# Optimization experiments

Hardware: AMD Instinct MI355X
Metric: run time of the kernel (lower is better)

Reference implementation:

```python
import jax, jax.numpy as jnp
import numpy as np

L = 24        # n_layer
E = 1024      # n_emb
H = 4 * E     # ffn hidden
V = 50277     # vocab
LN_EPS = 1e-5


def _ln(x, w, b):
    m = x.mean(-1, keepdims=True)
    v = ((x - m) ** 2).mean(-1, keepdims=True)
    return (x - m) / jnp.sqrt(v + LN_EPS) * w + b


def setup_inputs() -> dict:
    key = jax.random.key(0)
    ks = jax.random.split(key, 24)
    s = 1.0 / np.sqrt(E)      # keep matvec outputs O(1) so exp-recurrence is stable
    sh = 1.0 / np.sqrt(H)
    inp = {
        "emb":      jax.random.normal(ks[0], (V, E), jnp.float32) * 0.02,
        "ln0_w":    jnp.ones((E,), jnp.float32),
        "ln0_b":    jnp.zeros((E,), jnp.float32),
        "ln1_w":    jnp.ones((L, E), jnp.float32),
        "ln1_b":    jnp.zeros((L, E), jnp.float32),
        "att_tmk":  jax.random.uniform(ks[1], (L, E), jnp.float32),
        "att_tmv":  jax.random.uniform(ks[2], (L, E), jnp.float32),
        "att_tmr":  jax.random.uniform(ks[3], (L, E), jnp.float32),
        "att_tf":   jax.random.normal(ks[4], (L, E), jnp.float32) * 0.3,
        # checkpoint stores raw time_decay; loader applies -exp(.)
        "att_td":   -jnp.exp(jax.random.normal(ks[5], (L, E), jnp.float32) * 0.3),
        "att_kw":   jax.random.normal(ks[6], (L, E, E), jnp.float32) * s,
        "att_vw":   jax.random.normal(ks[7], (L, E, E), jnp.float32) * s,
        "att_rw":   jax.random.normal(ks[8], (L, E, E), jnp.float32) * s,
        "att_ow":   jax.random.normal(ks[9], (L, E, E), jnp.float32) * s,
        "ln2_w":    jnp.ones((L, E), jnp.float32),
        "ln2_b":    jnp.zeros((L, E), jnp.float32),
        "ffn_tmk":  jax.random.uniform(ks[10], (L, E), jnp.float32),
        "ffn_tmr":  jax.random.uniform(ks[11], (L, E), jnp.float32),
        "ffn_kw":   jax.random.normal(ks[12], (L, H, E), jnp.float32) * s,
        "ffn_vw":   jax.random.normal(ks[13], (L, E, H), jnp.float32) * sh,
        "ffn_rw":   jax.random.normal(ks[14], (L, E, E), jnp.float32) * s,
        "ln_out_w": jnp.ones((E,), jnp.float32),
        "ln_out_b": jnp.zeros((E,), jnp.float32),
        "head_w":   jax.random.normal(ks[15], (V, E), jnp.float32) * s,
        "token":    123,
    }
    state = jnp.zeros((5 * L, E), jnp.float32)
    state = state.at[4::5].set(-1e30)  # pp slot, as in empty_state()
    inp["state"] = state
    return inp


def _rwkv_forward(emb, ln0_w, ln0_b, ln1_w, ln1_b, att_tmk, att_tmv, att_tmr,
                  att_tf, att_td, att_kw, att_vw, att_rw, att_ow,
                  ln2_w, ln2_b, ffn_tmk, ffn_tmr, ffn_kw, ffn_vw, ffn_rw,
                  ln_out_w, ln_out_b, head_w, state, token):
    x = emb[token]
    x = _ln(x, ln0_w, ln0_b)           # blocks.0.ln0 applied once before layer 0
    st = state.reshape(L, 5, E)        # slots: (ffn_x, att_x, aa, bb, pp)

    def step(x, inp):
        (s, l1w, l1b, tmk, tmv, tmr, tf, td, kw, vw, rw, ow,
         l2w, l2b, ftmk, ftmr, fkw, fvw, frw) = inp
        ffn_x, att_x, aa, bb, pp = s[0], s[1], s[2], s[3], s[4]
        # --- time-mix (SA) ---
        xn = _ln(x, l1w, l1b)
        xk = xn * tmk + att_x * (1 - tmk)
        xv = xn * tmv + att_x * (1 - tmv)
        xr = xn * tmr + att_x * (1 - tmr)
        r = jax.nn.sigmoid(rw @ xr)
        k = kw @ xk
        v = vw @ xv
        # numerically-stabilized WKV output
        ww = tf + k
        p = jnp.maximum(pp, ww)
        e1 = jnp.exp(pp - p)
        e2 = jnp.exp(ww - p)
        a = e1 * aa + e2 * v
        b = e1 * bb + e2
        # state update
        ww2 = pp + td
        p2 = jnp.maximum(ww2, k)
        f1 = jnp.exp(ww2 - p2)
        f2 = jnp.exp(k - p2)
        naa = f1 * aa + f2 * v
        nbb = f1 * bb + f2
        npp = p2
        sx = x + ow @ (r * a / b)
        # --- channel-mix (FF) ---
        xn2 = _ln(sx, l2w, l2b)
        fxk = xn2 * ftmk + ffn_x * (1 - ftmk)
        fxr = xn2 * ftmr + ffn_x * (1 - ftmr)
        fr = jax.nn.sigmoid(frw @ fxr)
        fk = jnp.square(jax.nn.relu(fkw @ fxk))
        out = sx + fr * (fvw @ fk)
        new_s = jnp.stack([xn2, xn, naa, nbb, npp])
        return out, new_s

    xs = (st, ln1_w, ln1_b, att_tmk, att_tmv, att_tmr, att_tf, att_td,
          att_kw, att_vw, att_rw, att_ow, ln2_w, ln2_b, ffn_tmk, ffn_tmr,
          ffn_kw, ffn_vw, ffn_rw)
    x, new_st = jax.lax.scan(step, x, xs)
    logits = head_w @ _ln(x, ln_out_w, ln_out_b)
    return logits, new_st.reshape(5 * L, E)


def reference(emb, ln0_w, ln0_b, ln1_w, ln1_b, att_tmk, att_tmv, att_tmr,
              att_tf, att_td, att_kw, att_vw, att_rw, att_ow,
              ln2_w, ln2_b, ffn_tmk, ffn_tmr, ffn_kw, ffn_vw, ffn_rw,
              ln_out_w, ln_out_b, head_w, state, token):
    return _rwkv_forward(emb, ln0_w, ln0_b, ln1_w, ln1_b, att_tmk, att_tmv,
                         att_tmr, att_tf, att_td, att_kw, att_vw, att_rw,
                         att_ow, ln2_w, ln2_b, ffn_tmk, ffn_tmr, ffn_kw,
                         ffn_vw, ffn_rw, ln_out_w, ln_out_b, head_w,
                         state, token)
```

## Files before the change

kernel.cpp:

```cpp
#include <hip/hip_runtime.h>

#define E 1024
#define H 4096
#define NLAYER 24
#define V 50277
#define NB 256
#define NT 1024
#define LN_EPS 1e-5f

typedef unsigned long long u64;

#define R1O    0
#define R2O    16384
#define POOLO  32768
#define SXO    36864
#define SSXO   37888
#define FXRO   38912
#define REDO   39936
#define PARTO  39968
#define PART2O 39984
#define SMEMF  40000

struct Params {
  const float* emb;   const float* ln0_w; const float* ln0_b;
  const float* ln1_w; const float* ln1_b;
  const float* tmk;   const float* tmv;   const float* tmr;
  const float* tf;    const float* td;
  const float* kw;    const float* vw;    const float* rw;  const float* ow;
  const float* ln2_w; const float* ln2_b;
  const float* ftmk;  const float* ftmr;
  const float* fkw;   const float* fvw;   const float* frw;
  const float* lnow;  const float* lnob;  const float* headw;
  const float* st;    const int* tok;
  float* out; float* ws;
};

__device__ __forceinline__ void stg_tag(u64* p, float v, unsigned tag) {
  u64 w = ((u64)__float_as_uint(v) << 32) | (u64)tag;
  __hip_atomic_store(p, w, __ATOMIC_RELAXED, __HIP_MEMORY_SCOPE_AGENT);
}
__device__ __forceinline__ u64 ld_tag(const u64* p) {
  return __hip_atomic_load(p, __ATOMIC_RELAXED, __HIP_MEMORY_SCOPE_AGENT);
}
__device__ __forceinline__ float poll_tag(const u64* p, unsigned tag) {
  u64 w = ld_tag(p);
  while ((unsigned)w != tag) { __builtin_amdgcn_s_sleep(1); w = ld_tag(p); }
  return __uint_as_float((unsigned)(w >> 32));
}

__device__ __forceinline__ void wait_pf() {
  asm volatile("s_waitcnt vmcnt(0)" ::: "memory");
}

__device__ __forceinline__ void gload_lds16(const float* g, float* l) {
  __builtin_amdgcn_global_load_lds(
      (const __attribute__((address_space(1))) unsigned int*)(g),
      (__attribute__((address_space(3))) unsigned int*)(l), 16, 0, 0);
}
__device__ __forceinline__ void pf_row4k(const float* row, float* dst, int lane) {
#pragma unroll
  for (int c = 0; c < 4; ++c)
    gload_lds16(row + c * 256 + lane * 4, dst + c * 256);
}

__device__ __forceinline__ float warp_sum(float v) {
#pragma unroll
  for (int off = 32; off; off >>= 1) v += __shfl_down(v, off);
  return v;
}

__device__ __forceinline__ float2 ln_stats(float v, float* red) {
  float a = v, b = v * v;
#pragma unroll
  for (int off = 32; off; off >>= 1) { a += __shfl_xor(a, off); b += __shfl_xor(b, off); }
  const int wid = threadIdx.x >> 6, lane = threadIdx.x & 63;
  if (lane == 0) { red[2 * wid] = a; red[2 * wid + 1] = b; }
  __syncthreads();
  float s1 = 0.f, s2 = 0.f;
  const float2* r2 = (const float2*)red;
#pragma unroll
  for (int j = 0; j < 16; ++j) { float2 t = r2[j]; s1 += t.x; s2 += t.y; }
  float m = s1 * (1.f / E);
  return make_float2(m, s2 * (1.f / E) - m * m);
}

__device__ __forceinline__ float dot4(float4 a, float4 b) {
  return a.x * b.x + a.y * b.y + a.z * b.z + a.w * b.w;
}

__device__ __forceinline__ float dotlds(const float* wrow, const float* vec, int lane) {
  const float4* w4 = (const float4*)wrow;
  const float4* v4 = (const float4*)vec;
  float acc = 0.f;
#pragma unroll
  for (int p = 0; p < 4; ++p)
    acc += dot4(w4[lane + p * 64], v4[lane + p * 64]);
  return warp_sum(acc);
}

__device__ __forceinline__ float dot1024(const float* __restrict__ Wrow,
                                         const float* vec, int lane) {
  const float4* W4 = (const float4*)Wrow;
  const float4* v4 = (const float4*)vec;
  float acc = 0.f;
#pragma unroll
  for (int p = 0; p < 4; ++p)
    acc += dot4(W4[lane + p * 64], v4[lane + p * 64]);
  return warp_sum(acc);
}

__global__ __launch_bounds__(NT, 1) void rwkv_kernel(Params p) {
  const int tid = threadIdx.x, bid = blockIdx.x;
  const int lane = tid & 63, wid = tid >> 6;

  extern __shared__ float smem[];
  float* r1     = smem + R1O;
  float* r2     = smem + R2O;
  float* pool   = smem + POOLO;
  float* s_x    = smem + SXO;
  float* s_sx   = smem + SSXO;
  float* s_fxr  = smem + FXRO;
  float* s_red  = smem + REDO;
  float* s_part = smem + PARTO;
  float* s_part2= smem + PART2O;

  u64* tws = (u64*)p.ws;
  u64* tk  = tws;
  u64* tv  = tws + 2 * E;
  u64* tr  = tws + 4 * E;
  u64* tsx = tws + 6 * E;
  u64* tx  = tws + 8 * E;
  u64* tfk = tws + 10 * E;

  float* out_st = p.out + V;
  const int token = p.tok[0];

  const bool hasA = wid < 12;
  const int rA = bid * 12 + wid;
  const int matA = rA >> 10, rmA = rA & (E - 1);
  const int rloc = wid >> 2, kc = wid & 3;
  const int rowO = bid * 4 + rloc;
  float* wA = r1 + wid * 1024;
  float* wD = r2 + wid * 1024;

  if (hasA) {
    const float* W = (matA == 0 ? p.kw : matA == 1 ? p.vw : p.rw) + (size_t)rmA * E;
    pf_row4k(W, wA, lane);
  }

  {
    float v = p.emb[(size_t)token * E + tid];
    float2 mv = ln_stats(v, s_red);
    s_x[tid] = (v - mv.x) / sqrtf(mv.y + LN_EPS) * p.ln0_w[tid] + p.ln0_b[tid];
  }

  for (int l = 0; l < NLAYER; ++l) {
    const float* stl = p.st + (size_t)5 * l * E;
    float* ostl = out_st + (size_t)5 * l * E;
    const int par = l & 1;
    const unsigned tg = (unsigned)(l + 1);

    float xv_;
    if (l > 0) { xv_ = poll_tag(&tx[par * E + tid], (unsigned)l); s_x[tid] = xv_; }
    else       { xv_ = s_x[tid]; }
    {
      float2 mv = ln_stats(xv_, s_red);
      float xn = (xv_ - mv.x) / sqrtf(mv.y + LN_EPS) * p.ln1_w[l * E + tid] + p.ln1_b[l * E + tid];
      float ax = stl[E + tid];
      float a = p.tmk[l * E + tid], b = p.tmv[l * E + tid], c = p.tmr[l * E + tid];
      pool[tid]        = xn * a + ax * (1.f - a);
      pool[1024 + tid] = xn * b + ax * (1.f - b);
      pool[2048 + tid] = xn * c + ax * (1.f - c);
      if (bid == 0) ostl[E + tid] = xn;
    }
    __syncthreads();
    wait_pf();
    if (hasA) {
      float d = dotlds(wA, pool + matA * 1024, lane);
      if (lane == 0) {
        u64* dst = (matA == 0 ? tk : matA == 1 ? tv : tr) + par * E + rmA;
        stg_tag(dst, matA == 2 ? 1.f / (1.f + expf(-d)) : d, tg);
      }
    }

    float4 wow = ((const float4*)(p.ow + (size_t)l * E * E + (size_t)rowO * E + kc * 256))[lane];
    pf_row4k(p.fkw + (size_t)l * H * E + (size_t)(bid * 16 + wid) * E, wA, lane);
    {
      const u64 *bk = tk + par * E + tid, *bv = tv + par * E + tid, *br = tr + par * E + tid;
      u64 wk = ld_tag(bk), wv = ld_tag(bv), wr = ld_tag(br);
      while ((unsigned)wk != tg) { __builtin_amdgcn_s_sleep(1); wk = ld_tag(bk); }
      while ((unsigned)wv != tg) { __builtin_amdgcn_s_sleep(1); wv = ld_tag(bv); }
      while ((unsigned)wr != tg) { __builtin_amdgcn_s_sleep(1); wr = ld_tag(br); }
      float kk = __uint_as_float((unsigned)(wk >> 32));
      float vv = __uint_as_float((unsigned)(wv >> 32));
      float rr = __uint_as_float((unsigned)(wr >> 32));
      float aav = stl[2 * E + tid], bbv = stl[3 * E + tid], ppv = stl[4 * E + tid];
      float tfv = p.tf[l * E + tid], tdv = p.td[l * E + tid];
      float wwv = tfv + kk;
      float pm = fmaxf(ppv, wwv);
      float e1 = expf(ppv - pm), e2 = expf(wwv - pm);
      float a = e1 * aav + e2 * vv, b = e1 * bbv + e2;
      pool[3072 + tid] = rr * a / b;
      float ww2 = ppv + tdv;
      float p2 = fmaxf(ww2, kk);
      float f1 = expf(ww2 - p2), f2 = expf(kk - p2);
      if (bid == 0) {
        ostl[2 * E + tid] = f1 * aav + f2 * vv;
        ostl[3 * E + tid] = f1 * bbv + f2;
        ostl[4 * E + tid] = p2;
      }
    }
    __syncthreads();
    {
      const float4* v4 = (const float4*)(pool + 3072 + kc * 256);
      float acc = warp_sum(dot4(wow, v4[lane]));
      if (lane == 0) s_part[wid] = acc;
    }
    __syncthreads();
    if (tid < 4) {
      float dsum = s_part[tid * 4] + s_part[tid * 4 + 1] +
                   s_part[tid * 4 + 2] + s_part[tid * 4 + 3];
      stg_tag(&tsx[par * E + bid * 4 + tid], s_x[bid * 4 + tid] + dsum, tg);
    }

    {
      float sxv = poll_tag(&tsx[par * E + tid], tg);
      s_sx[tid] = sxv;
      float4 wfr = ((const float4*)(p.frw + (size_t)l * E * E + (size_t)rowO * E + kc * 256))[lane];
      pf_row4k(p.fvw + (size_t)l * E * H + (size_t)rowO * H + kc * 1024, wD, lane);
      float2 mv = ln_stats(sxv, s_red);
      float xn2 = (sxv - mv.x) / sqrtf(mv.y + LN_EPS) * p.ln2_w[l * E + tid] + p.ln2_b[l * E + tid];
      float fx = stl[tid];
      float a = p.ftmk[l * E + tid], b = p.ftmr[l * E + tid];
      pool[tid]  = xn2 * a + fx * (1.f - a);
      s_fxr[tid] = xn2 * b + fx * (1.f - b);
      if (bid == 0) ostl[tid] = xn2;
      __syncthreads();
      float d = dotlds(wA, pool, lane);
      if (lane == 0) { float t = fmaxf(d, 0.f); stg_tag(&tfk[par * H + bid * 16 + wid], t * t, tg); }
      const float4* f4 = (const float4*)(s_fxr + kc * 256);
      float fp = warp_sum(dot4(wfr, f4[lane]));
      if (lane == 0) s_part2[wid] = fp;
    }

    if (l + 1 < NLAYER && hasA) {
      const float* W = (matA == 0 ? p.kw : matA == 1 ? p.vw : p.rw) +
                       (size_t)(l + 1) * E * E + (size_t)rmA * E;
      pf_row4k(W, wA, lane);
    }
    __syncthreads();
    {
      const u64* base = tfk + par * H;
      u64 w0 = ld_tag(base + tid);
      u64 w1 = ld_tag(base + tid + 1024);
      u64 w2 = ld_tag(base + tid + 2048);
      u64 w3 = ld_tag(base + tid + 3072);
      while ((unsigned)w0 != tg) { __builtin_amdgcn_s_sleep(1); w0 = ld_tag(base + tid); }
      while ((unsigned)w1 != tg) { __builtin_amdgcn_s_sleep(1); w1 = ld_tag(base + tid + 1024); }
      while ((unsigned)w2 != tg) { __builtin_amdgcn_s_sleep(1); w2 = ld_tag(base + tid + 2048); }
      while ((unsigned)w3 != tg) { __builtin_amdgcn_s_sleep(1); w3 = ld_tag(base + tid + 3072); }
      pool[tid]        = __uint_as_float((unsigned)(w0 >> 32));
      pool[tid + 1024] = __uint_as_float((unsigned)(w1 >> 32));
      pool[tid + 2048] = __uint_as_float((unsigned)(w2 >> 32));
      pool[tid + 3072] = __uint_as_float((unsigned)(w3 >> 32));
    }
    __syncthreads();
    {
      const float4* v4 = (const float4*)(pool + kc * 1024);
      const float4* w4 = (const float4*)wD;
      float acc = 0.f;
#pragma unroll
      for (int pc = 0; pc < 4; ++pc)
        acc += dot4(w4[lane + pc * 64], v4[lane + pc * 64]);
      acc = warp_sum(acc);
      if (lane == 0) s_part[wid] = acc;
    }
    __syncthreads();
    if (tid < 4) {
      float dsum = s_part[tid * 4] + s_part[tid * 4 + 1] +
                   s_part[tid * 4 + 2] + s_part[tid * 4 + 3];
      float frs  = s_part2[tid * 4] + s_part2[tid * 4 + 1] +
                   s_part2[tid * 4 + 2] + s_part2[tid * 4 + 3];
      float fr = 1.f / (1.f + expf(-frs));
      stg_tag(&tx[((l + 1) & 1) * E + bid * 4 + tid],
              s_sx[bid * 4 + tid] + fr * dsum, tg);
    }
  }

  {
    float xv_ = poll_tag(&tx[(NLAYER & 1) * E + tid], (unsigned)NLAYER);
    float2 mv = ln_stats(xv_, s_red);
    pool[tid] = (xv_ - mv.x) / sqrtf(mv.y + LN_EPS) * p.lnow[tid] + p.lnob[tid];
  }
  __syncthreads();
  {
    const int gw = bid * 16 + wid;
    for (int row = gw; row < V; row += 4096) {
      float d = dot1024(p.headw + (size_t)row * E, pool, lane);
      if (lane == 0) p.out[row] = d;
    }
  }
}

extern "C" void kernel_launch(void* const* d_in, const int* in_sizes, int n_in,
                              void* d_out, int out_size, void* d_ws, size_t ws_size,
                              hipStream_t stream) {
  Params p;
  p.emb   = (const float*)d_in[0];
  p.ln0_w = (const float*)d_in[1];
  p.ln0_b = (const float*)d_in[2];
  p.ln1_w = (const float*)d_in[3];
  p.ln1_b = (const float*)d_in[4];
  p.tmk   = (const float*)d_in[5];
  p.tmv   = (const float*)d_in[6];
  p.tmr   = (const float*)d_in[7];
  p.tf    = (const float*)d_in[8];
  p.td    = (const float*)d_in[9];
  p.kw    = (const float*)d_in[10];
  p.vw    = (const float*)d_in[11];
  p.rw    = (const float*)d_in[12];
  p.ow    = (const float*)d_in[13];
  p.ln2_w = (const float*)d_in[14];
  p.ln2_b = (const float*)d_in[15];
  p.ftmk  = (const float*)d_in[16];
  p.ftmr  = (const float*)d_in[17];
  p.fkw   = (const float*)d_in[18];
  p.fvw   = (const float*)d_in[19];
  p.frw   = (const float*)d_in[20];
  p.lnow  = (const float*)d_in[21];
  p.lnob  = (const float*)d_in[22];
  p.headw = (const float*)d_in[23];
  if (in_sizes[24] == 1) {
    p.tok = (const int*)d_in[24];
    p.st  = (const float*)d_in[25];
  } else {
    p.st  = (const float*)d_in[24];
    p.tok = (const int*)d_in[25];
  }
  p.out   = (float*)d_out;
  p.ws    = (float*)d_ws;

  hipMemsetAsync(d_ws, 0, (10 * E + 2 * H) * sizeof(unsigned long long), stream);

  void* args[] = { &p };
  hipLaunchCooperativeKernel((const void*)rwkv_kernel, dim3(NB), dim3(NT),
                             args, SMEMF * sizeof(float), stream);
}
```

Before: 579.2 us.

## Assign whole output rows to single warps, removing cross-warp partial reductions

Each row of the ow, frw and fvw matvecs is now computed by one warp instead of four warps each taking a quarter of the row. The quarter-row partial sums went through shared memory and needed extra __syncthreads. Removing them cuts barrier count per layer, and the next-layer kvr weight prefetch moves into the tfk polling phase. The cost is that fewer warps do the ow, frw and fvw dot products, so per-warp work rises: fvw runs 4 warps over 4096 elements each. Some parameter loads are also hoisted ahead of the LN reductions.

```diff
diff --git a/kernel.cpp b/kernel.cpp
--- a/kernel.cpp
+++ b/kernel.cpp
@@ -17,9 +17,8 @@
 #define SSXO   37888
 #define FXRO   38912
 #define REDO   39936
-#define PARTO  39968
-#define PART2O 39984
-#define SMEMF  40000
+#define FRO    39968
+#define SMEMF  39972
 
 struct Params {
   const float* emb;   const float* ln0_w; const float* ln0_b;
@@ -114,15 +113,14 @@
   const int lane = tid & 63, wid = tid >> 6;
 
   extern __shared__ float smem[];
-  float* r1     = smem + R1O;
-  float* r2     = smem + R2O;
-  float* pool   = smem + POOLO;
-  float* s_x    = smem + SXO;
-  float* s_sx   = smem + SSXO;
-  float* s_fxr  = smem + FXRO;
-  float* s_red  = smem + REDO;
-  float* s_part = smem + PARTO;
-  float* s_part2= smem + PART2O;
+  float* r1    = smem + R1O;
+  float* r2    = smem + R2O;
+  float* pool  = smem + POOLO;
+  float* s_x   = smem + SXO;
+  float* s_sx  = smem + SSXO;
+  float* s_fxr = smem + FXRO;
+  float* s_red = smem + REDO;
+  float* s_fr  = smem + FRO;
 
   u64* tws = (u64*)p.ws;
   u64* tk  = tws;
@@ -139,9 +137,11 @@
   const int rA = bid * 12 + wid;
   const int matA = rA >> 10, rmA = rA & (E - 1);
   const int rloc = wid >> 2, kc = wid & 3;
-  const int rowO = bid * 4 + rloc;
+  const bool isRowW = wid < 4;
+  const int rowW = bid * 4 + wid;
+  const bool isFrw = wid >= 4 && wid < 8;
+  const int rowF = bid * 4 + (wid - 4);
   float* wA = r1 + wid * 1024;
-  float* wD = r2 + wid * 1024;
 
   if (hasA) {
     const float* W = (matA == 0 ? p.kw : matA == 1 ? p.vw : p.rw) + (size_t)rmA * E;
@@ -164,10 +164,11 @@
     if (l > 0) { xv_ = poll_tag(&tx[par * E + tid], (unsigned)l); s_x[tid] = xv_; }
     else       { xv_ = s_x[tid]; }
     {
-      float2 mv = ln_stats(xv_, s_red);
-      float xn = (xv_ - mv.x) / sqrtf(mv.y + LN_EPS) * p.ln1_w[l * E + tid] + p.ln1_b[l * E + tid];
+      float l1w = p.ln1_w[l * E + tid], l1b = p.ln1_b[l * E + tid];
       float ax = stl[E + tid];
       float a = p.tmk[l * E + tid], b = p.tmv[l * E + tid], c = p.tmr[l * E + tid];
+      float2 mv = ln_stats(xv_, s_red);
+      float xn = (xv_ - mv.x) / sqrtf(mv.y + LN_EPS) * l1w + l1b;
       pool[tid]        = xn * a + ax * (1.f - a);
       pool[1024 + tid] = xn * b + ax * (1.f - b);
       pool[2048 + tid] = xn * c + ax * (1.f - c);
@@ -183,8 +184,6 @@
       }
     }
 
-    float4 wow = ((const float4*)(p.ow + (size_t)l * E * E + (size_t)rowO * E + kc * 256))[lane];
-    pf_row4k(p.fkw + (size_t)l * H * E + (size_t)(bid * 16 + wid) * E, wA, lane);
     {
       const u64 *bk = tk + par * E + tid, *bv = tv + par * E + tid, *br = tr + par * E + tid;
       u64 wk = ld_tag(bk), wv = ld_tag(bv), wr = ld_tag(br);
@@ -196,6 +195,12 @@
       float rr = __uint_as_float((unsigned)(wr >> 32));
       float aav = stl[2 * E + tid], bbv = stl[3 * E + tid], ppv = stl[4 * E + tid];
       float tfv = p.tf[l * E + tid], tdv = p.td[l * E + tid];
+      float4 wow0, wow1, wow2, wow3;
+      if (isRowW) {
+        const float4* W4 = (const float4*)(p.ow + (size_t)l * E * E + (size_t)rowW * E);
+        wow0 = W4[lane]; wow1 = W4[lane + 64]; wow2 = W4[lane + 128]; wow3 = W4[lane + 192];
+      }
+      pf_row4k(p.fkw + (size_t)l * H * E + (size_t)(bid * 16 + wid) * E, wA, lane);
       float wwv = tfv + kk;
       float pm = fmaxf(ppv, wwv);
       float e1 = expf(ppv - pm), e2 = expf(wwv - pm);
@@ -209,45 +214,46 @@
         ostl[3 * E + tid] = f1 * bbv + f2;
         ostl[4 * E + tid] = p2;
       }
-    }
-    __syncthreads();
-    {
-      const float4* v4 = (const float4*)(pool + 3072 + kc * 256);
-      float acc = warp_sum(dot4(wow, v4[lane]));
-      if (lane == 0) s_part[wid] = acc;
-    }
-    __syncthreads();
-    if (tid < 4) {
-      float dsum = s_part[tid * 4] + s_part[tid * 4 + 1] +
-                   s_part[tid * 4 + 2] + s_part[tid * 4 + 3];
-      stg_tag(&tsx[par * E + bid * 4 + tid], s_x[bid * 4 + tid] + dsum, tg);
+      __syncthreads();
+      if (isRowW) {
+        const float4* v4 = (const float4*)(pool + 3072);
+        float acc = dot4(wow0, v4[lane]) + dot4(wow1, v4[lane + 64]) +
+                    dot4(wow2, v4[lane + 128]) + dot4(wow3, v4[lane + 192]);
+        acc = warp_sum(acc);
+        if (lane == 0) stg_tag(&tsx[par * E + rowW], s_x[rowW] + acc, tg);
+      }
     }
 
     {
       float sxv = poll_tag(&tsx[par * E + tid], tg);
       s_sx[tid] = sxv;
-      float4 wfr = ((const float4*)(p.frw + (size_t)l * E * E + (size_t)rowO * E + kc * 256))[lane];
-      pf_row4k(p.fvw + (size_t)l * E * H + (size_t)rowO * H + kc * 1024, wD, lane);
-      float2 mv = ln_stats(sxv, s_red);
-      float xn2 = (sxv - mv.x) / sqrtf(mv.y + LN_EPS) * p.ln2_w[l * E + tid] + p.ln2_b[l * E + tid];
+      float l2w = p.ln2_w[l * E + tid], l2b = p.ln2_b[l * E + tid];
       float fx = stl[tid];
       float a = p.ftmk[l * E + tid], b = p.ftmr[l * E + tid];
+      float4 wfr0, wfr1, wfr2, wfr3;
+      if (isFrw) {
+        const float4* F4 = (const float4*)(p.frw + (size_t)l * E * E + (size_t)rowF * E);
+        wfr0 = F4[lane]; wfr1 = F4[lane + 64]; wfr2 = F4[lane + 128]; wfr3 = F4[lane + 192];
+      }
+      pf_row4k(p.fvw + (size_t)l * E * H + (size_t)(bid * 4 + rloc) * H + kc * 1024,
+               r2 + rloc * 4096 + kc * 1024, lane);
+      float2 mv = ln_stats(sxv, s_red);
+      float xn2 = (sxv - mv.x) / sqrtf(mv.y + LN_EPS) * l2w + l2b;
       pool[tid]  = xn2 * a + fx * (1.f - a);
       s_fxr[tid] = xn2 * b + fx * (1.f - b);
       if (bid == 0) ostl[tid] = xn2;
       __syncthreads();
       float d = dotlds(wA, pool, lane);
       if (lane == 0) { float t = fmaxf(d, 0.f); stg_tag(&tfk[par * H + bid * 16 + wid], t * t, tg); }
-      const float4* f4 = (const float4*)(s_fxr + kc * 256);
-      float fp = warp_sum(dot4(wfr, f4[lane]));
-      if (lane == 0) s_part2[wid] = fp;
-    }
-
-    if (l + 1 < NLAYER && hasA) {
-      const float* W = (matA == 0 ? p.kw : matA == 1 ? p.vw : p.rw) +
-                       (size_t)(l + 1) * E * E + (size_t)rmA * E;
-      pf_row4k(W, wA, lane);
-    }
+      if (isFrw) {
+        const float4* f4 = (const float4*)s_fxr;
+        float acc = dot4(wfr0, f4[lane]) + dot4(wfr1, f4[lane + 64]) +
+                    dot4(wfr2, f4[lane + 128]) + dot4(wfr3, f4[lane + 192]);
+        acc = warp_sum(acc);
+        if (lane == 0) s_fr[wid - 4] = acc;
+      }
+    }
+
     __syncthreads();
     {
       const u64* base = tfk + par * H;
@@ -263,27 +269,25 @@
       pool[tid + 1024] = __uint_as_float((unsigned)(w1 >> 32));
       pool[tid + 2048] = __uint_as_float((unsigned)(w2 >> 32));
       pool[tid + 3072] = __uint_as_float((unsigned)(w3 >> 32));
+      if (l + 1 < NLAYER && hasA) {
+        const float* W = (matA == 0 ? p.kw : matA == 1 ? p.vw : p.rw) +
+                         (size_t)(l + 1) * E * E + (size_t)rmA * E;
+        pf_row4k(W, wA, lane);
+      }
     }
     __syncthreads();
-    {
-      const float4* v4 = (const float4*)(pool + kc * 1024);
-      const float4* w4 = (const float4*)wD;
+    if (isRowW) {
+      const float4* w4 = (const float4*)(r2 + wid * 4096);
+      const float4* v4 = (const float4*)pool;
       float acc = 0.f;
 #pragma unroll
-      for (int pc = 0; pc < 4; ++pc)
+      for (int pc = 0; pc < 16; ++pc)
         acc += dot4(w4[lane + pc * 64], v4[lane + pc * 64]);
       acc = warp_sum(acc);
-      if (lane == 0) s_part[wid] = acc;
-    }
-    __syncthreads();
-    if (tid < 4) {
-      float dsum = s_part[tid * 4] + s_part[tid * 4 + 1] +
-                   s_part[tid * 4 + 2] + s_part[tid * 4 + 3];
-      float frs  = s_part2[tid * 4] + s_part2[tid * 4 + 1] +
-                   s_part2[tid * 4 + 2] + s_part2[tid * 4 + 3];
-      float fr = 1.f / (1.f + expf(-frs));
-      stg_tag(&tx[((l + 1) & 1) * E + bid * 4 + tid],
-              s_sx[bid * 4 + tid] + fr * dsum, tg);
+      if (lane == 0) {
+        float fr = 1.f / (1.f + expf(-s_fr[wid]));
+        stg_tag(&tx[((l + 1) & 1) * E + rowW], s_sx[rowW] + fr * acc, tg);
+      }
     }
   }
 
```

Measured after the change: 768.3 us. 32.7% more time.
